# Kernel tuning notes

Hardware: AMD Instinct MI355X
Metric: run time of the kernel (lower is better)

The kernel has to match this reference:

```python
import jax, jax.numpy as jnp
import numpy as np
import math

B, L, E, H, FF = 8, 1024, 1024, 16, 4096
DH = E // H  # 64
EPS = 1e-10


def layer_norm(x, gamma, beta):
    mean = jnp.mean(x, axis=-1, keepdims=True)
    var = jnp.mean((x - mean) ** 2, axis=-1, keepdims=True)
    return gamma * (x - mean) / jnp.sqrt(var + EPS) + beta


def setup_inputs() -> dict:
    key = jax.random.key(0)
    ks = jax.random.split(key, 16)
    c_qk = math.sqrt(6.0 / (E + DH))
    c_o = math.sqrt(6.0 / (H * DH + E))
    c1 = math.sqrt(6.0 / (E + FF))
    c2 = math.sqrt(6.0 / (FF + E))
    u = lambda k, shp, c: jax.random.uniform(k, shp, jnp.float32, -c, c)
    return {
        "x": jax.random.normal(ks[0], (B, L, E), jnp.float32),
        # per-head projections stacked: [H, E, DH] (stored input-major = W^T of torch Linear)
        "Wq": u(ks[1], (H, E, DH), c_qk), "bq": jnp.zeros((H, DH), jnp.float32),
        "Wk": u(ks[2], (H, E, DH), c_qk), "bk": jnp.zeros((H, DH), jnp.float32),
        "Wv": u(ks[3], (H, E, DH), c_qk), "bv": jnp.zeros((H, DH), jnp.float32),
        "Wo": u(ks[4], (H * DH, E), c_o), "bo": jnp.zeros((E,), jnp.float32),
        "W1": u(ks[5], (E, FF), c1), "b1": jnp.zeros((FF,), jnp.float32),
        "W2": u(ks[6], (FF, E), c2), "b2": jnp.zeros((E,), jnp.float32),
        "gamma1": jnp.ones((E,), jnp.float32), "beta1": jnp.zeros((E,), jnp.float32),
        "gamma2": jnp.ones((E,), jnp.float32), "beta2": jnp.zeros((E,), jnp.float32),
    }


def reference(x, Wq, bq, Wk, bk, Wv, bv, Wo, bo, W1, b1, W2, b2, gamma1, beta1, gamma2, beta2):
    # multi-head attention (all heads batched; concat order == head order)
    q = jnp.einsum("ble,hed->bhld", x, Wq) + bq[None, :, None, :]
    k = jnp.einsum("ble,hed->bhld", x, Wk) + bk[None, :, None, :]
    v = jnp.einsum("ble,hed->bhld", x, Wv) + bv[None, :, None, :]
    scores = jnp.einsum("bhld,bhmd->bhlm", q, k) / math.sqrt(DH)
    weights = jax.nn.softmax(scores, axis=-1)
    y = jnp.einsum("bhlm,bhmd->bhld", weights, v)          # [B,H,L,DH]
    concat = y.transpose(0, 2, 1, 3).reshape(B, L, H * DH)  # [B,L,E]
    out1 = concat @ Wo + bo
    # residual + LN (dropout p=0 -> identity)
    out2 = layer_norm(out1 + x, gamma1, beta1)
    # FFN
    out3 = jax.nn.relu(out2 @ W1 + b1) @ W2 + b2
    return layer_norm(out3 + out2, gamma2, beta2)
```

## Files before the change

kernel.cpp:

```cpp
#include <hip/hip_runtime.h>
#include <hip/hip_bf16.h>

#define BB 8
#define LL 1024
#define EE 1024
#define HH 16
#define DHH 64
#define FFF 4096

typedef __attribute__((ext_vector_type(8))) short short8;
typedef __attribute__((ext_vector_type(4))) float f32x4;

__device__ inline f32x4 mfma16(short8 a, short8 b, f32x4 c) {
    return __builtin_amdgcn_mfma_f32_16x16x32_bf16(a, b, c, 0, 0, 0);
}

__device__ inline void async_ld16(const __hip_bfloat16* g, __hip_bfloat16* l) {
    __builtin_amdgcn_global_load_lds(
        (const __attribute__((address_space(1))) void*)g,
        (__attribute__((address_space(3))) void*)l, 16, 0, 0);
}

__device__ inline unsigned short bf16bits(float f) {
    __hip_bfloat16 h = __float2bfloat16(f);
    return *reinterpret_cast<unsigned short*>(&h);
}

__device__ inline float bf2f(unsigned short u) {
    unsigned v = ((unsigned)u) << 16;
    return *reinterpret_cast<float*>(&v);
}

__device__ inline float exp2_fast(float x) {
    float r;
    asm("v_exp_f32 %0, %1" : "=v"(r) : "v"(x));
    return r;
}

__device__ inline unsigned cvt_pk_bf16(float lo, float hi) {
    unsigned r;
    asm("v_cvt_pk_bf16_f32 %0, %1, %2" : "=v"(r) : "v"(lo), "v"(hi));
    return r;
}

__device__ inline void wg_barrier() {
    asm volatile("" ::: "memory");
    __builtin_amdgcn_s_barrier();
    asm volatile("" ::: "memory");
}

__global__ __launch_bounds__(256) void cvt_bf16(const float* __restrict__ in,
                                                __hip_bfloat16* __restrict__ out) {
    size_t i = (size_t)blockIdx.x * 256 + threadIdx.x;
    float4 v = reinterpret_cast<const float4*>(in)[i];
    ushort4 o;
    o.x = bf16bits(v.x); o.y = bf16bits(v.y); o.z = bf16bits(v.z); o.w = bf16bits(v.w);
    reinterpret_cast<ushort4*>(out)[i] = o;
}

__global__ __launch_bounds__(256) void wtrans(const float* __restrict__ src,
                                              __hip_bfloat16* __restrict__ dst,
                                              int K, int N, long src_z, long dst_z) {
    src += (size_t)blockIdx.z * src_z;
    dst += (size_t)blockIdx.z * dst_z;
    __shared__ __hip_bfloat16 t[64 * 66];
    const int k0 = blockIdx.x * 64, n0 = blockIdx.y * 64;
    const int tid = threadIdx.x;
#pragma unroll
    for (int i = 0; i < 16; ++i) {
        int idx = tid + i * 256;
        int kr = idx >> 6, nc = idx & 63;
        t[kr * 66 + nc] = __float2bfloat16(src[(size_t)(k0 + kr) * N + n0 + nc]);
    }
    __syncthreads();
#pragma unroll
    for (int i = 0; i < 16; ++i) {
        int idx = tid + i * 256;
        int nr = idx >> 6, kc = idx & 63;
        dst[(size_t)(n0 + nr) * K + k0 + kc] = t[kc * 66 + nr];
    }
}

__global__ __launch_bounds__(256) void vtrans(const __hip_bfloat16* __restrict__ qkv,
                                              __hip_bfloat16* __restrict__ vt) {
    const int bh = blockIdx.x, lt = blockIdx.y;
    const int b = bh >> 4, h = bh & 15;
    __shared__ __hip_bfloat16 t[64 * 66];
    const int tid = threadIdx.x;
#pragma unroll
    for (int i = 0; i < 16; ++i) {
        int idx = tid + i * 256;
        int lr = idx >> 6, d = idx & 63;
        t[lr * 66 + d] = qkv[(size_t)(b * LL + lt * 64 + lr) * 3072 + 2048 + h * 64 + d];
    }
    __syncthreads();
#pragma unroll
    for (int i = 0; i < 16; ++i) {
        int idx = tid + i * 256;
        int dr = idx >> 6, lc = idx & 63;
        vt[((size_t)bh * 64 + dr) * LL + lt * 64 + lc] = t[lc * 66 + dr];
    }
}

template <int MODE, int CM, int CN, int ZX>
__global__ __launch_bounds__(512, 2) void gemm256(
    const __hip_bfloat16* __restrict__ A, const __hip_bfloat16* __restrict__ Bm,
    int M, int N, int K, int ksplit, size_t zstride, void* __restrict__ Cout,
    const float* __restrict__ bias0, const float* __restrict__ bias1,
    const float* __restrict__ bias2) {
    __shared__ __hip_bfloat16 lds[2][2][2][128 * 64];
    const int flat = blockIdx.x + gridDim.x * (blockIdx.y + gridDim.y * blockIdx.z);
    const int xcd = flat & 7, rank = flat >> 3;
    const int mc = xcd & 3, hc = xcd >> 2;
    const int ml = rank / CN, nl = rank % CN;
    const int mb = mc * CM + ml;
    const int nb = ZX ? nl : (hc * CN + nl);
    const int zb = ZX ? hc : 0;
    const int m0 = mb * 256, n0 = nb * 256;
    const int tid = threadIdx.x;
    const int wid = tid >> 6, l = tid & 63;
    const int wm = wid >> 2, wn = wid & 3;
    const int lr = l & 15, lg = l >> 4;
    const int T = K / (64 * ksplit);
    const int kb = zb * T;

    const int c0 = tid, c1 = tid + 512;
    const int r0 = c0 >> 3, s0 = (((c0 & 7) ^ (r0 & 7)) << 3);
    const int r1 = c1 >> 3, s1 = (((c1 & 7) ^ (r1 & 7)) << 3);
    const int ldst0 = wid * 512;
    const int ldst1 = 4096 + wid * 512;

#define STAGE(bi, isb, half, kt)                                                   \
    do {                                                                           \
        const __hip_bfloat16* _s = (isb) ? Bm : A;                                 \
        const int _br = ((isb) ? n0 : m0) + (half) * 128;                          \
        __hip_bfloat16* _d = &lds[bi][isb][half][0];                               \
        async_ld16(_s + (size_t)(_br + r0) * K + (size_t)(kb + (kt)) * 64 + s0, _d + ldst0); \
        async_ld16(_s + (size_t)(_br + r1) * K + (size_t)(kb + (kt)) * 64 + s1, _d + ldst1); \
    } while (0)

    f32x4 acc[8][4];
#pragma unroll
    for (int m = 0; m < 8; ++m)
#pragma unroll
        for (int n = 0; n < 4; ++n) acc[m][n] = (f32x4){0.f, 0.f, 0.f, 0.f};

    short8 aR[4][2], bR[4][2];

#define LDA(dst, bi, m, kh)                                                        \
    do {                                                                           \
        const int _ra = (m) * 16 + lr;                                             \
        const int _sl = ((kh) * 4 + lg) ^ (_ra & 7);                               \
        dst = *reinterpret_cast<const short8*>(&lds[bi][0][wm][_ra * 64 + _sl * 8]); \
    } while (0)
#define LDB(dst, bi, n, kh)                                                        \
    do {                                                                           \
        const int _rb = (wn & 1) * 64 + (n) * 16 + lr;                             \
        const int _sl = ((kh) * 4 + lg) ^ (_rb & 7);                               \
        dst = *reinterpret_cast<const short8*>(&lds[bi][1][wn >> 1][_rb * 64 + _sl * 8]); \
    } while (0)

    STAGE(0, 1, 0, 0);
    STAGE(0, 0, 0, 0);
    STAGE(0, 1, 1, 0);
    STAGE(0, 0, 1, 0);
    if (T > 1) {
        STAGE(1, 1, 0, 1);
        STAGE(1, 0, 0, 1);
        asm volatile("s_waitcnt vmcnt(4)" ::: "memory");
    } else {
        asm volatile("s_waitcnt vmcnt(0)" ::: "memory");
    }
    wg_barrier();

    for (int t = 0; t < T; ++t) {
        const int cur = t & 1, nxt = cur ^ 1;
#pragma unroll
        for (int m = 0; m < 4; ++m) {
            LDA(aR[m][0], cur, m, 0);
            LDA(aR[m][1], cur, m, 1);
        }
#pragma unroll
        for (int n = 0; n < 2; ++n) {
            LDB(bR[n][0], cur, n, 0);
            LDB(bR[n][1], cur, n, 1);
        }
        if (t + 1 < T) STAGE(nxt, 1, 1, t + 1);
        wg_barrier();
        __builtin_amdgcn_s_setprio(1);
#pragma unroll
        for (int m = 0; m < 4; ++m)
#pragma unroll
            for (int n = 0; n < 2; ++n) {
                acc[m][n] = mfma16(aR[m][0], bR[n][0], acc[m][n]);
                acc[m][n] = mfma16(aR[m][1], bR[n][1], acc[m][n]);
            }
        __builtin_amdgcn_s_setprio(0);
        wg_barrier();
#pragma unroll
        for (int n = 2; n < 4; ++n) {
            LDB(bR[n][0], cur, n, 0);
            LDB(bR[n][1], cur, n, 1);
        }
        if (t + 1 < T) STAGE(nxt, 0, 1, t + 1);
        wg_barrier();
        __builtin_amdgcn_s_setprio(1);
#pragma unroll
        for (int m = 0; m < 4; ++m)
#pragma unroll
            for (int n = 2; n < 4; ++n) {
                acc[m][n] = mfma16(aR[m][0], bR[n][0], acc[m][n]);
                acc[m][n] = mfma16(aR[m][1], bR[n][1], acc[m][n]);
            }
        __builtin_amdgcn_s_setprio(0);
        wg_barrier();
#pragma unroll
        for (int m = 0; m < 4; ++m) {
            LDA(aR[m][0], cur, m + 4, 0);
            LDA(aR[m][1], cur, m + 4, 1);
        }
        if (t + 2 < T) STAGE(cur, 1, 0, t + 2);
        wg_barrier();
        __builtin_amdgcn_s_setprio(1);
#pragma unroll
        for (int m = 0; m < 4; ++m)
#pragma unroll
            for (int n = 0; n < 2; ++n) {
                acc[m + 4][n] = mfma16(aR[m][0], bR[n][0], acc[m + 4][n]);
                acc[m + 4][n] = mfma16(aR[m][1], bR[n][1], acc[m + 4][n]);
            }
        __builtin_amdgcn_s_setprio(0);
        wg_barrier();
        if (t + 2 < T) STAGE(cur, 0, 0, t + 2);
        wg_barrier();
        __builtin_amdgcn_s_setprio(1);
#pragma unroll
        for (int m = 0; m < 4; ++m)
#pragma unroll
            for (int n = 2; n < 4; ++n) {
                acc[m + 4][n] = mfma16(aR[m][0], bR[n][0], acc[m + 4][n]);
                acc[m + 4][n] = mfma16(aR[m][1], bR[n][1], acc[m + 4][n]);
            }
        __builtin_amdgcn_s_setprio(0);
        if (t + 2 < T)
            asm volatile("s_waitcnt vmcnt(4)" ::: "memory");
        else
            asm volatile("s_waitcnt vmcnt(0)" ::: "memory");
        wg_barrier();
    }
#undef STAGE
#undef LDA
#undef LDB

    __syncthreads();
    float* eb = reinterpret_cast<float*>(&lds[0][0][0][0]) + wid * (16 * 68);
    const int erow = l >> 3, ec = l & 7;
    const int rowg = m0 + wm * 128;
    const int colg = n0 + wn * 64;
    float bv[4];
#pragma unroll
    for (int n = 0; n < 4; ++n) {
        if constexpr (MODE == 0) {
            const int col = colg + n * 16 + lr;
            int s = col >> 10;
            const float* bp = (s == 0) ? bias0 : ((s == 1) ? bias1 : bias2);
            bv[n] = bp[col & 1023];
        } else if constexpr (MODE == 2) {
            bv[n] = bias0[colg + n * 16 + lr];
        } else {
            bv[n] = 0.f;
        }
    }
    __hip_bfloat16* Cb = (MODE == 4)
        ? ((__hip_bfloat16*)Cout + (size_t)zb * zstride)
        : (__hip_bfloat16*)Cout;
#pragma unroll
    for (int m = 0; m < 8; ++m) {
#pragma unroll
        for (int n = 0; n < 4; ++n)
#pragma unroll
            for (int r = 0; r < 4; ++r) {
                float v = acc[m][n][r] + bv[n];
                if constexpr (MODE == 2) v = fmaxf(v, 0.f);
                eb[(lg * 4 + r) * 68 + n * 16 + lr] = v;
            }
#pragma unroll
        for (int i = 0; i < 2; ++i) {
            const int rr = erow + i * 8;
            float4 v0 = *reinterpret_cast<float4*>(&eb[rr * 68 + ec * 8]);
            float4 v1 = *reinterpret_cast<float4*>(&eb[rr * 68 + ec * 8 + 4]);
            uint4 o;
            o.x = cvt_pk_bf16(v0.x, v0.y);
            o.y = cvt_pk_bf16(v0.z, v0.w);
            o.z = cvt_pk_bf16(v1.x, v1.y);
            o.w = cvt_pk_bf16(v1.z, v1.w);
            *reinterpret_cast<uint4*>(&Cb[(size_t)(rowg + m * 16 + rr) * N + colg + ec * 8]) = o;
        }
    }
}

__global__ __launch_bounds__(512) void attn3(const __hip_bfloat16* __restrict__ qkv,
                                             const __hip_bfloat16* __restrict__ vt,
                                             __hip_bfloat16* __restrict__ cat) {
    const int orig = blockIdx.y * 8 + blockIdx.x;
    const int swz = (orig & 7) * 128 + (orig >> 3);
    const int qt = swz & 7, bh = swz >> 3;
    const int b = bh >> 4, h = bh & 15;
    const int tid = threadIdx.x, w = tid >> 6, l = tid & 63;
    const int lr = l & 15, lg = l >> 4;
    const int sw = lr & 7;

    __shared__ __hip_bfloat16 Ks[2][64 * 64];
    __shared__ __hip_bfloat16 Vs[2][64 * 64];
    __shared__ __hip_bfloat16 plds[8][16 * 72];

    const size_t qrow = (size_t)(b * LL + qt * 128 + w * 16 + lr);
    const short8 qa0 = *reinterpret_cast<const short8*>(qkv + qrow * 3072 + h * 64 + lg * 8);
    const short8 qa1 = *reinterpret_cast<const short8*>(qkv + qrow * 3072 + h * 64 + 32 + lg * 8);

    const int rA = tid >> 3, sA = (((tid & 7) ^ (rA & 7)) << 3);
    const __hip_bfloat16* kg = qkv + (size_t)(b * LL + rA) * 3072 + 1024 + h * 64 + sA;
    const __hip_bfloat16* vg = vt + ((size_t)bh * 64 + rA) * LL + sA;

#define STAGE_KV(bi, k0)                                      \
    do {                                                      \
        async_ld16(kg + (size_t)(k0) * 3072, &Ks[bi][w * 512]); \
        async_ld16(vg + (k0), &Vs[bi][w * 512]);              \
    } while (0)

    float mrun = -INFINITY, lrun = 0.f;
    f32x4 oacc[4];
#pragma unroll
    for (int n = 0; n < 4; ++n) oacc[n] = (f32x4){0.f, 0.f, 0.f, 0.f};

    STAGE_KV(0, 0);
    asm volatile("s_waitcnt vmcnt(0)" ::: "memory");
    __syncthreads();

    const float SCALE = 0.18033688011112042f;

    int cur = 0;
    for (int kt = 0; kt < 16; ++kt) {
        if (kt < 15) STAGE_KV(cur ^ 1, (kt + 1) * 64);

        f32x4 s[4];
#pragma unroll
        for (int m = 0; m < 4; ++m) {
            const int krow = m * 16 + lr;
            const short8 kf0 =
                *reinterpret_cast<const short8*>(&Ks[cur][krow * 64 + ((lg ^ sw) << 3)]);
            const short8 kf1 =
                *reinterpret_cast<const short8*>(&Ks[cur][krow * 64 + (((lg + 4) ^ sw) << 3)]);
            f32x4 t = (f32x4){0.f, 0.f, 0.f, 0.f};
            t = mfma16(kf0, qa0, t);
            t = mfma16(kf1, qa1, t);
            s[m] = t * SCALE;
        }
        float smax = s[0][0];
#pragma unroll
        for (int m = 0; m < 4; ++m)
#pragma unroll
            for (int r = 0; r < 4; ++r) smax = fmaxf(smax, s[m][r]);
        smax = fmaxf(smax, __shfl_xor(smax, 16, 64));
        smax = fmaxf(smax, __shfl_xor(smax, 32, 64));
        if (__any(smax > mrun + 8.0f)) {
            const float mnew = fmaxf(mrun, smax);
            const float alpha = exp2_fast(mrun - mnew);
            mrun = mnew;
            lrun *= alpha;
#pragma unroll
            for (int r = 0; r < 4; ++r) {
                const float aD = __shfl(alpha, lg * 4 + r, 64);
#pragma unroll
                for (int n = 0; n < 4; ++n) oacc[n][r] *= aD;
            }
        }
        float p[4][4];
        float tsum = 0.f;
#pragma unroll
        for (int m = 0; m < 4; ++m)
#pragma unroll
            for (int r = 0; r < 4; ++r) {
                p[m][r] = exp2_fast(s[m][r] - mrun);
                tsum += p[m][r];
            }
        tsum += __shfl_xor(tsum, 16, 64);
        tsum += __shfl_xor(tsum, 32, 64);
        lrun += tsum;

#pragma unroll
        for (int m = 0; m < 4; ++m) {
            uint2 d;
            d.x = cvt_pk_bf16(p[m][0], p[m][1]);
            d.y = cvt_pk_bf16(p[m][2], p[m][3]);
            *reinterpret_cast<uint2*>(&plds[w][lr * 72 + m * 16 + lg * 4]) = d;
        }
        asm volatile("s_waitcnt lgkmcnt(0)" ::: "memory");
        __builtin_amdgcn_sched_barrier(0);

        const short8 pa0 = *reinterpret_cast<const short8*>(&plds[w][lr * 72 + lg * 8]);
        const short8 pa1 = *reinterpret_cast<const short8*>(&plds[w][lr * 72 + 32 + lg * 8]);
#pragma unroll
        for (int n = 0; n < 4; ++n) {
            const int vrow = n * 16 + lr;
            const short8 vf0 =
                *reinterpret_cast<const short8*>(&Vs[cur][vrow * 64 + ((lg ^ sw) << 3)]);
            const short8 vf1 =
                *reinterpret_cast<const short8*>(&Vs[cur][vrow * 64 + (((lg + 4) ^ sw) << 3)]);
            oacc[n] = mfma16(pa0, vf0, oacc[n]);
            oacc[n] = mfma16(pa1, vf1, oacc[n]);
        }

        asm volatile("s_waitcnt vmcnt(0)" ::: "memory");
        __syncthreads();
        cur ^= 1;
    }
#undef STAGE_KV

    float rinv[4];
#pragma unroll
    for (int r = 0; r < 4; ++r) rinv[r] = 1.0f / __shfl(lrun, lg * 4 + r, 64);
#pragma unroll
    for (int n = 0; n < 4; ++n)
#pragma unroll
        for (int r = 0; r < 4; ++r) {
            const float v = oacc[n][r] * rinv[r];
            cat[(size_t)(b * LL + qt * 128 + w * 16 + lg * 4 + r) * EE + h * 64 + n * 16 + lr] =
                __float2bfloat16(v);
        }
}

__global__ __launch_bounds__(256) void ln_fused(const __hip_bfloat16* __restrict__ a,
                                                const __hip_bfloat16* __restrict__ b,
                                                const float* __restrict__ c,
                                                const float* __restrict__ colbias,
                                                const float* __restrict__ gamma,
                                                const float* __restrict__ beta,
                                                float* __restrict__ outf,
                                                __hip_bfloat16* __restrict__ outb) {
    const int row = blockIdx.x, tid = threadIdx.x;
    const size_t base = (size_t)row * EE;
    const ushort4 ua = reinterpret_cast<const ushort4*>(a + base)[tid];
    const ushort4 ub = reinterpret_cast<const ushort4*>(b + base)[tid];
    float4 z = reinterpret_cast<const float4*>(c + base)[tid];
    float4 cb = reinterpret_cast<const float4*>(colbias)[tid];
    float4 x;
    x.x = bf2f(ua.x) + bf2f(ub.x) + z.x + cb.x;
    x.y = bf2f(ua.y) + bf2f(ub.y) + z.y + cb.y;
    x.z = bf2f(ua.z) + bf2f(ub.z) + z.z + cb.z;
    x.w = bf2f(ua.w) + bf2f(ub.w) + z.w + cb.w;
    float s = x.x + x.y + x.z + x.w;
    float s2 = x.x * x.x + x.y * x.y + x.z * x.z + x.w * x.w;
#pragma unroll
    for (int msk = 1; msk < 64; msk <<= 1) {
        s += __shfl_xor(s, msk, 64);
        s2 += __shfl_xor(s2, msk, 64);
    }
    __shared__ float red[8];
    const int w = tid >> 6, l = tid & 63;
    if (l == 0) { red[w] = s; red[4 + w] = s2; }
    __syncthreads();
    s = red[0] + red[1] + red[2] + red[3];
    s2 = red[4] + red[5] + red[6] + red[7];
    const float mean = s * (1.f / 1024.f);
    const float var = s2 * (1.f / 1024.f) - mean * mean;
    const float rstd = rsqrtf(var + 1e-10f);
    float4 g = reinterpret_cast<const float4*>(gamma)[tid];
    float4 bt = reinterpret_cast<const float4*>(beta)[tid];
    float4 o;
    o.x = g.x * (x.x - mean) * rstd + bt.x;
    o.y = g.y * (x.y - mean) * rstd + bt.y;
    o.z = g.z * (x.z - mean) * rstd + bt.z;
    o.w = g.w * (x.w - mean) * rstd + bt.w;
    reinterpret_cast<float4*>(outf + base)[tid] = o;
    if (outb) {
        ushort4 ob;
        ob.x = bf16bits(o.x); ob.y = bf16bits(o.y); ob.z = bf16bits(o.z); ob.w = bf16bits(o.w);
        reinterpret_cast<ushort4*>(outb + base)[tid] = ob;
    }
}

extern "C" void kernel_launch(void* const* d_in, const int* in_sizes, int n_in,
                              void* d_out, int out_size, void* d_ws, size_t ws_size,
                              hipStream_t stream) {
    const float* x = (const float*)d_in[0];
    const float* Wq = (const float*)d_in[1];
    const float* bq = (const float*)d_in[2];
    const float* Wk = (const float*)d_in[3];
    const float* bk = (const float*)d_in[4];
    const float* Wv = (const float*)d_in[5];
    const float* bv = (const float*)d_in[6];
    const float* Wo = (const float*)d_in[7];
    const float* bo = (const float*)d_in[8];
    const float* W1 = (const float*)d_in[9];
    const float* b1 = (const float*)d_in[10];
    const float* W2 = (const float*)d_in[11];
    const float* b2 = (const float*)d_in[12];
    const float* gamma1 = (const float*)d_in[13];
    const float* beta1 = (const float*)d_in[14];
    const float* gamma2 = (const float*)d_in[15];
    const float* beta2 = (const float*)d_in[16];
    float* out = (float*)d_out;

    char* Wb = (char*)d_ws;
    const size_t MB = (size_t)1 << 20;
    if (ws_size < 168 * MB) return;
    __hip_bfloat16* xb = (__hip_bfloat16*)(Wb + 0 * MB);
    __hip_bfloat16* wqkvt = (__hip_bfloat16*)(Wb + 16 * MB);
    __hip_bfloat16* wot = (__hip_bfloat16*)(Wb + 22 * MB);
    __hip_bfloat16* w1t = (__hip_bfloat16*)(Wb + 24 * MB);
    __hip_bfloat16* w2t = (__hip_bfloat16*)(Wb + 32 * MB);
    __hip_bfloat16* qkvb = (__hip_bfloat16*)(Wb + 40 * MB);
    __hip_bfloat16* vtb = (__hip_bfloat16*)(Wb + 88 * MB);
    __hip_bfloat16* catb = (__hip_bfloat16*)(Wb + 104 * MB);
    __hip_bfloat16* p0 = (__hip_bfloat16*)(Wb + 40 * MB);
    float* out2f = (float*)(Wb + 104 * MB);
    __hip_bfloat16* out2b = (__hip_bfloat16*)(Wb + 136 * MB);
    __hip_bfloat16* hbuf = (__hip_bfloat16*)(Wb + 40 * MB);
    __hip_bfloat16* q0 = (__hip_bfloat16*)(Wb + 0 * MB);
    const size_t PSTRIDE = (size_t)8192 * 1024;

    cvt_bf16<<<8192, 256, 0, stream>>>(x, xb);
    wtrans<<<dim3(16, 1, 16), 256, 0, stream>>>(Wq, wqkvt, 1024, 64, 65536, 65536);
    wtrans<<<dim3(16, 1, 16), 256, 0, stream>>>(Wk, wqkvt + 1024 * 1024, 1024, 64, 65536, 65536);
    wtrans<<<dim3(16, 1, 16), 256, 0, stream>>>(Wv, wqkvt + 2048 * 1024, 1024, 64, 65536, 65536);
    wtrans<<<dim3(16, 16, 1), 256, 0, stream>>>(Wo, wot, 1024, 1024, 0, 0);
    wtrans<<<dim3(16, 64, 1), 256, 0, stream>>>(W1, w1t, 1024, 4096, 0, 0);
    wtrans<<<dim3(64, 16, 1), 256, 0, stream>>>(W2, w2t, 4096, 1024, 0, 0);
    gemm256<0, 8, 6, 0><<<dim3(32, 12, 1), 512, 0, stream>>>(xb, wqkvt, 8192, 3072, 1024, 1, 0,
                                                             qkvb, bq, bk, bv);
    vtrans<<<dim3(128, 16), 256, 0, stream>>>(qkvb, vtb);
    attn3<<<dim3(8, 128), 512, 0, stream>>>(qkvb, vtb, catb);
    gemm256<4, 8, 4, 1><<<dim3(32, 4, 2), 512, 0, stream>>>(catb, wot, 8192, 1024, 1024, 2,
                                                            PSTRIDE, p0, nullptr, nullptr,
                                                            nullptr);
    ln_fused<<<8192, 256, 0, stream>>>(p0, p0 + PSTRIDE, x, bo, gamma1, beta1, out2f, out2b);
    gemm256<2, 8, 8, 0><<<dim3(32, 16, 1), 512, 0, stream>>>(out2b, w1t, 8192, 4096, 1024, 1, 0,
                                                             hbuf, b1, nullptr, nullptr);
    gemm256<4, 8, 4, 1><<<dim3(32, 4, 2), 512, 0, stream>>>(hbuf, w2t, 8192, 1024, 4096, 2,
                                                            PSTRIDE, q0, nullptr, nullptr,
                                                            nullptr);
    ln_fused<<<8192, 256, 0, stream>>>(q0, q0 + PSTRIDE, out2f, b2, gamma2, beta2, out, nullptr);
}
```

Measured before the change: 335.4 us.

## Use 4-wave 256-thread GEMM blocks with 128x128 per-wave tiles

```diff
diff --git a/kernel.cpp b/kernel.cpp
--- a/kernel.cpp
+++ b/kernel.cpp
@@ -103,7 +103,7 @@
 }
 
 template <int MODE, int CM, int CN, int ZX>
-__global__ __launch_bounds__(512, 2) void gemm256(
+__global__ __launch_bounds__(256, 1) void gemm256(
     const __hip_bfloat16* __restrict__ A, const __hip_bfloat16* __restrict__ Bm,
     int M, int N, int K, int ksplit, size_t zstride, void* __restrict__ Cout,
     const float* __restrict__ bias0, const float* __restrict__ bias1,
@@ -119,55 +119,58 @@
     const int m0 = mb * 256, n0 = nb * 256;
     const int tid = threadIdx.x;
     const int wid = tid >> 6, l = tid & 63;
-    const int wm = wid >> 2, wn = wid & 3;
+    const int wm = wid >> 1, wn = wid & 1;
     const int lr = l & 15, lg = l >> 4;
     const int T = K / (64 * ksplit);
     const int kb = zb * T;
 
-    const int c0 = tid, c1 = tid + 512;
-    const int r0 = c0 >> 3, s0 = (((c0 & 7) ^ (r0 & 7)) << 3);
-    const int r1 = c1 >> 3, s1 = (((c1 & 7) ^ (r1 & 7)) << 3);
-    const int ldst0 = wid * 512;
-    const int ldst1 = 4096 + wid * 512;
-
-#define STAGE(bi, isb, half, kt)                                                   \
-    do {                                                                           \
-        const __hip_bfloat16* _s = (isb) ? Bm : A;                                 \
-        const int _br = ((isb) ? n0 : m0) + (half) * 128;                          \
-        __hip_bfloat16* _d = &lds[bi][isb][half][0];                               \
-        async_ld16(_s + (size_t)(_br + r0) * K + (size_t)(kb + (kt)) * 64 + s0, _d + ldst0); \
-        async_ld16(_s + (size_t)(_br + r1) * K + (size_t)(kb + (kt)) * 64 + s1, _d + ldst1); \
+    const int srow = l >> 3;
+    const int gslot8 = (((l & 7) ^ srow) << 3);
+
+#define STAGE(bi, isb, half, kt)                                                     \
+    do {                                                                             \
+        const __hip_bfloat16* _s = (isb) ? Bm : A;                                   \
+        const int _br = ((isb) ? n0 : m0) + (half) * 128;                            \
+        __hip_bfloat16* _d = &lds[bi][isb][half][0];                                 \
+        _Pragma("unroll")                                                            \
+        for (int _j = 0; _j < 4; ++_j) {                                             \
+            const int _ins = wid * 4 + _j;                                           \
+            async_ld16(_s + (size_t)(_br + _ins * 8 + srow) * K +                    \
+                           (size_t)(kb + (kt)) * 64 + gslot8,                        \
+                       _d + _ins * 512);                                             \
+        }                                                                            \
     } while (0)
 
-    f32x4 acc[8][4];
+    f32x4 acc[8][8];
 #pragma unroll
     for (int m = 0; m < 8; ++m)
 #pragma unroll
-        for (int n = 0; n < 4; ++n) acc[m][n] = (f32x4){0.f, 0.f, 0.f, 0.f};
-
-    short8 aR[4][2], bR[4][2];
-
-#define LDA(dst, bi, m, kh)                                                        \
-    do {                                                                           \
-        const int _ra = (m) * 16 + lr;                                             \
-        const int _sl = ((kh) * 4 + lg) ^ (_ra & 7);                               \
+        for (int n = 0; n < 8; ++n) acc[m][n] = (f32x4){0.f, 0.f, 0.f, 0.f};
+
+    short8 aR[4][2], bR[8][2];
+
+#define LDA(dst, bi, m, kh)                                                          \
+    do {                                                                             \
+        const int _ra = (m) * 16 + lr;                                               \
+        const int _sl = ((kh) * 4 + lg) ^ (_ra & 7);                                 \
         dst = *reinterpret_cast<const short8*>(&lds[bi][0][wm][_ra * 64 + _sl * 8]); \
     } while (0)
-#define LDB(dst, bi, n, kh)                                                        \
-    do {                                                                           \
-        const int _rb = (wn & 1) * 64 + (n) * 16 + lr;                             \
-        const int _sl = ((kh) * 4 + lg) ^ (_rb & 7);                               \
-        dst = *reinterpret_cast<const short8*>(&lds[bi][1][wn >> 1][_rb * 64 + _sl * 8]); \
+#define LDB(dst, bi, n, kh)                                                          \
+    do {                                                                             \
+        const int _rb = (n) * 16 + lr;                                               \
+        const int _sl = ((kh) * 4 + lg) ^ (_rb & 7);                                 \
+        dst = *reinterpret_cast<const short8*>(&lds[bi][1][wn][_rb * 64 + _sl * 8]); \
     } while (0)
 
     STAGE(0, 1, 0, 0);
+    STAGE(0, 1, 1, 0);
     STAGE(0, 0, 0, 0);
-    STAGE(0, 1, 1, 0);
     STAGE(0, 0, 1, 0);
     if (T > 1) {
         STAGE(1, 1, 0, 1);
+        STAGE(1, 1, 1, 1);
         STAGE(1, 0, 0, 1);
-        asm volatile("s_waitcnt vmcnt(4)" ::: "memory");
+        asm volatile("s_waitcnt vmcnt(12)" ::: "memory");
     } else {
         asm volatile("s_waitcnt vmcnt(0)" ::: "memory");
     }
@@ -181,34 +184,33 @@
             LDA(aR[m][1], cur, m, 1);
         }
 #pragma unroll
-        for (int n = 0; n < 2; ++n) {
+        for (int n = 0; n < 4; ++n) {
             LDB(bR[n][0], cur, n, 0);
             LDB(bR[n][1], cur, n, 1);
         }
-        if (t + 1 < T) STAGE(nxt, 1, 1, t + 1);
+        if (t + 1 < T) STAGE(nxt, 0, 1, t + 1);
         wg_barrier();
         __builtin_amdgcn_s_setprio(1);
 #pragma unroll
         for (int m = 0; m < 4; ++m)
 #pragma unroll
-            for (int n = 0; n < 2; ++n) {
+            for (int n = 0; n < 4; ++n) {
                 acc[m][n] = mfma16(aR[m][0], bR[n][0], acc[m][n]);
                 acc[m][n] = mfma16(aR[m][1], bR[n][1], acc[m][n]);
             }
         __builtin_amdgcn_s_setprio(0);
         wg_barrier();
 #pragma unroll
-        for (int n = 2; n < 4; ++n) {
+        for (int n = 4; n < 8; ++n) {
             LDB(bR[n][0], cur, n, 0);
             LDB(bR[n][1], cur, n, 1);
         }
-        if (t + 1 < T) STAGE(nxt, 0, 1, t + 1);
         wg_barrier();
         __builtin_amdgcn_s_setprio(1);
 #pragma unroll
         for (int m = 0; m < 4; ++m)
 #pragma unroll
-            for (int n = 2; n < 4; ++n) {
+            for (int n = 4; n < 8; ++n) {
                 acc[m][n] = mfma16(aR[m][0], bR[n][0], acc[m][n]);
                 acc[m][n] = mfma16(aR[m][1], bR[n][1], acc[m][n]);
             }
@@ -225,25 +227,28 @@
 #pragma unroll
         for (int m = 0; m < 4; ++m)
 #pragma unroll
-            for (int n = 0; n < 2; ++n) {
+            for (int n = 4; n < 8; ++n) {
                 acc[m + 4][n] = mfma16(aR[m][0], bR[n][0], acc[m + 4][n]);
                 acc[m + 4][n] = mfma16(aR[m][1], bR[n][1], acc[m + 4][n]);
             }
         __builtin_amdgcn_s_setprio(0);
         wg_barrier();
-        if (t + 2 < T) STAGE(cur, 0, 0, t + 2);
+        if (t + 2 < T) {
+            STAGE(cur, 1, 1, t + 2);
+            STAGE(cur, 0, 0, t + 2);
+        }
         wg_barrier();
         __builtin_amdgcn_s_setprio(1);
 #pragma unroll
         for (int m = 0; m < 4; ++m)
 #pragma unroll
-            for (int n = 2; n < 4; ++n) {
+            for (int n = 0; n < 4; ++n) {
                 acc[m + 4][n] = mfma16(aR[m][0], bR[n][0], acc[m + 4][n]);
                 acc[m + 4][n] = mfma16(aR[m][1], bR[n][1], acc[m + 4][n]);
             }
         __builtin_amdgcn_s_setprio(0);
         if (t + 2 < T)
-            asm volatile("s_waitcnt vmcnt(4)" ::: "memory");
+            asm volatile("s_waitcnt vmcnt(12)" ::: "memory");
         else
             asm volatile("s_waitcnt vmcnt(0)" ::: "memory");
         wg_barrier();
@@ -253,13 +258,13 @@
 #undef LDB
 
     __syncthreads();
-    float* eb = reinterpret_cast<float*>(&lds[0][0][0][0]) + wid * (16 * 68);
-    const int erow = l >> 3, ec = l & 7;
+    float* eb = reinterpret_cast<float*>(&lds[0][0][0][0]) + wid * (16 * 132);
+    const int ec = l & 15, er = l >> 4;
     const int rowg = m0 + wm * 128;
-    const int colg = n0 + wn * 64;
-    float bv[4];
-#pragma unroll
-    for (int n = 0; n < 4; ++n) {
+    const int colg = n0 + wn * 128;
+    float bv[8];
+#pragma unroll
+    for (int n = 0; n < 8; ++n) {
         if constexpr (MODE == 0) {
             const int col = colg + n * 16 + lr;
             int s = col >> 10;
@@ -277,18 +282,18 @@
 #pragma unroll
     for (int m = 0; m < 8; ++m) {
 #pragma unroll
-        for (int n = 0; n < 4; ++n)
+        for (int n = 0; n < 8; ++n)
 #pragma unroll
             for (int r = 0; r < 4; ++r) {
                 float v = acc[m][n][r] + bv[n];
                 if constexpr (MODE == 2) v = fmaxf(v, 0.f);
-                eb[(lg * 4 + r) * 68 + n * 16 + lr] = v;
-            }
-#pragma unroll
-        for (int i = 0; i < 2; ++i) {
-            const int rr = erow + i * 8;
-            float4 v0 = *reinterpret_cast<float4*>(&eb[rr * 68 + ec * 8]);
-            float4 v1 = *reinterpret_cast<float4*>(&eb[rr * 68 + ec * 8 + 4]);
+                eb[(lg * 4 + r) * 132 + n * 16 + lr] = v;
+            }
+#pragma unroll
+        for (int i = 0; i < 4; ++i) {
+            const int rr = er + i * 4;
+            float4 v0 = *reinterpret_cast<float4*>(&eb[rr * 132 + ec * 8]);
+            float4 v1 = *reinterpret_cast<float4*>(&eb[rr * 132 + ec * 8 + 4]);
             uint4 o;
             o.x = cvt_pk_bf16(v0.x, v0.y);
             o.y = cvt_pk_bf16(v0.z, v0.w);
@@ -527,17 +532,17 @@
     wtrans<<<dim3(16, 16, 1), 256, 0, stream>>>(Wo, wot, 1024, 1024, 0, 0);
     wtrans<<<dim3(16, 64, 1), 256, 0, stream>>>(W1, w1t, 1024, 4096, 0, 0);
     wtrans<<<dim3(64, 16, 1), 256, 0, stream>>>(W2, w2t, 4096, 1024, 0, 0);
-    gemm256<0, 8, 6, 0><<<dim3(32, 12, 1), 512, 0, stream>>>(xb, wqkvt, 8192, 3072, 1024, 1, 0,
+    gemm256<0, 8, 6, 0><<<dim3(32, 12, 1), 256, 0, stream>>>(xb, wqkvt, 8192, 3072, 1024, 1, 0,
                                                              qkvb, bq, bk, bv);
     vtrans<<<dim3(128, 16), 256, 0, stream>>>(qkvb, vtb);
     attn3<<<dim3(8, 128), 512, 0, stream>>>(qkvb, vtb, catb);
-    gemm256<4, 8, 4, 1><<<dim3(32, 4, 2), 512, 0, stream>>>(catb, wot, 8192, 1024, 1024, 2,
+    gemm256<4, 8, 4, 1><<<dim3(32, 4, 2), 256, 0, stream>>>(catb, wot, 8192, 1024, 1024, 2,
                                                             PSTRIDE, p0, nullptr, nullptr,
                                                             nullptr);
     ln_fused<<<8192, 256, 0, stream>>>(p0, p0 + PSTRIDE, x, bo, gamma1, beta1, out2f, out2b);
-    gemm256<2, 8, 8, 0><<<dim3(32, 16, 1), 512, 0, stream>>>(out2b, w1t, 8192, 4096, 1024, 1, 0,
+    gemm256<2, 8, 8, 0><<<dim3(32, 16, 1), 256, 0, stream>>>(out2b, w1t, 8192, 4096, 1024, 1, 0,
                                                              hbuf, b1, nullptr, nullptr);
-    gemm256<4, 8, 4, 1><<<dim3(32, 4, 2), 512, 0, stream>>>(hbuf, w2t, 8192, 1024, 4096, 2,
+    gemm256<4, 8, 4, 1><<<dim3(32, 4, 2), 256, 0, stream>>>(hbuf, w2t, 8192, 1024, 4096, 2,
                                                             PSTRIDE, q0, nullptr, nullptr,
                                                             nullptr);
     ln_fused<<<8192, 256, 0, stream>>>(q0, q0 + PSTRIDE, out2f, b2, gamma2, beta2, out, nullptr);
```

Measured after the change: 353.3 us. 5.3% more time.
